# Optimization experiments

Hardware: AMD Instinct MI355X
Metric: run time of the kernel (lower is better)

The kernel has to match this reference:

```python
import jax, jax.numpy as jnp
import numpy as np

B, R, C, E, H = 2, 190, 512, 256, 8  # batch, pair-rows, alignment cols, embed, heads
D = E // H  # head_dim = 32; head_qk_dim = 1 since qk_dim == nb_heads


def setup_inputs() -> dict:
    key = jax.random.key(0)
    ks = jax.random.split(key, 6)
    s = 0.02
    return {
        "x": jax.random.normal(ks[0], (B, R, C, E), dtype=jnp.float32),
        "Wq": jax.random.normal(ks[1], (H, E), dtype=jnp.float32) * s,
        "bq": jnp.zeros((H,), dtype=jnp.float32),
        "Wk": jax.random.normal(ks[2], (H, E), dtype=jnp.float32) * s,
        "bk": jnp.zeros((H,), dtype=jnp.float32),
        "Wv": jax.random.normal(ks[3], (E, E), dtype=jnp.float32) * s,
        "bv": jnp.zeros((E,), dtype=jnp.float32),
        "Wo": jax.random.normal(ks[4], (E, E), dtype=jnp.float32) * s,
        "bo": jnp.zeros((E,), dtype=jnp.float32),
    }


def reference(x, Wq, bq, Wk, bk, Wv, bv, Wo, bo):
    b, r, c, e = x.shape
    h = Wq.shape[0]
    d = e // h
    # q,k projections: qk_dim == nb_heads, so per-head qk feature dim is 1.
    # Shapes: [b,r,h,c] (head axis before the col axis, matching transpose(2,3)).
    q = jnp.einsum('brce,he->brhc', x, Wq) + bq[:, None]
    k = jnp.einsum('brce,he->brhc', x, Wk) + bk[:, None]
    # v: [b,r,h,c,d]
    v = (jnp.einsum('brce,fe->brcf', x, Wv) + bv).reshape(b, r, c, h, d)
    v = jnp.transpose(v, (0, 1, 3, 2, 4))
    # elu+1 feature map, then normalize over the col (sequence) axis
    q = jax.nn.elu(q) + 1.0
    k = jax.nn.elu(k) + 1.0
    q = q / jnp.mean(q, axis=-1, keepdims=True)
    k = k / jnp.sum(k, axis=-1, keepdims=True)
    # KtV: k^T @ v with qk head-dim 1 -> [b,r,h,d]
    ktv = jnp.einsum('brhc,brhcd->brhd', k, v)
    # q @ KtV -> [b,r,c,h,d], flatten heads back to embed dim
    V = jnp.einsum('brhc,brhd->brchd', q, ktv).reshape(b, r, c, e)
    out = jnp.einsum('brce,fe->brcf', V, Wo) + bo
    return out
```

## Files before the change

kernel.cpp:

```cpp
#include <hip/hip_runtime.h>
#include <stdint.h>

#define PAIRS  380
#define CDIM   512
#define EDIM   256
#define HDIM   8
#define DDIM   32
#define CHUNK  64
#define NCHUNK 8
#define XSTR   260
#define NSPLIT 4
#define CPS    2

#define Q_OFF      0
#define MSH_OFF    4096
#define YP_OFF     6144
#define QS_OFF     14336
#define KS_OFF     14368
#define SCR_FLOATS 14400
#define OUT_STRIDE 131072

__device__ __forceinline__ float bf2f(uint16_t u) {
  union { uint32_t i; float f; } v; v.i = ((uint32_t)u) << 16; return v.f;
}
__device__ __forceinline__ uint16_t f2bf(float f) {
  union { float f; uint32_t i; } v; v.f = f;
  return (uint16_t)((v.i + 0x7FFFu + ((v.i >> 16) & 1u)) >> 16);
}

__device__ __forceinline__ float4 ld4(const void* p, size_t idx, int f32) {
  if (f32) return ((const float4*)p)[idx >> 2];
  ushort4 u = *(const ushort4*)((const uint16_t*)p + idx);
  return make_float4(bf2f(u.x), bf2f(u.y), bf2f(u.z), bf2f(u.w));
}
__device__ __forceinline__ float ld1(const void* p, size_t idx, int f32) {
  return f32 ? ((const float*)p)[idx] : bf2f(((const uint16_t*)p)[idx]);
}

__global__ void sniff_all(const uint16_t* p0, const uint16_t* p1, const uint16_t* p2,
                          const uint16_t* p3, const uint16_t* p4, const uint16_t* p5,
                          const uint16_t* p6, const uint16_t* p7, const uint16_t* p8,
                          int n0, int n1, int n2, int n3, int n4, int n5, int n6,
                          int n7, int n8, int* __restrict__ flags) {
  const uint16_t* ps[9] = {p0, p1, p2, p3, p4, p5, p6, p7, p8};
  const int       ns[9] = {n0, n1, n2, n3, n4, n5, n6, n7, n8};
  __shared__ int sf;
  const int tid = threadIdx.x;
  #pragma unroll
  for (int j = 0; j < 9; ++j) {
    if (tid == 0) sf = 0;
    __syncthreads();
    const uint16_t* p = ps[j];
    int lim = ns[j] < 4096 ? ns[j] : 4096;
    int huge = 0;
    for (int i = tid; i < lim; i += 256) {
      int e = (p[i] >> 7) & 0xFF;
      huge |= (e >= 0xA0);
    }
    if (huge) atomicOr(&sf, 1);
    __syncthreads();
    if (tid == 0) flags[j] = sf;
    __syncthreads();
  }
}

__global__ void __launch_bounds__(256, 2)
sla_phase1(const void* __restrict__ xg,
           const void* __restrict__ Wq, const void* __restrict__ bq,
           const void* __restrict__ Wk, const void* __restrict__ bk,
           const int* __restrict__ flags,
           float* __restrict__ scratch, long long sstride)
{
  const int fx = flags[0], fwq = flags[1], fbq = flags[2];
  const int fwk = flags[3], fbk = flags[4];

  __shared__ __align__(16) uint16_t xs[CHUNK][XSTR];
  __shared__ __align__(16) float    wqk[16][EDIM];
  __shared__ __align__(16) float    kc[CHUNK][HDIM];

  const int tid  = threadIdx.x;
  const int pair = blockIdx.x / NSPLIT;
  const int sp   = blockIdx.x % NSPLIT;
  const size_t xbase = (size_t)pair * (CDIM * EDIM);
  float* sbase = scratch + (size_t)pair * (size_t)sstride;

  for (int i = tid; i < 16 * EDIM / 4; i += 256) {
    int row = i >> 6;
    int col = (i & 63) << 2;
    float4 w = (row < 8) ? ld4(Wq, (size_t)row * EDIM + col, fwq)
                         : ld4(Wk, (size_t)(row - 8) * EDIM + col, fwk);
    *(float4*)&wqk[row][col] = w;
  }

  const int t  = tid >> 6;
  const int cl = tid & 63;
  const int h0 = (t & 1) * 4;
  const void* bsrc = (t < 2) ? bq : bk;
  const int   fb   = (t < 2) ? fbq : fbk;
  const float bias0 = ld1(bsrc, h0 + 0, fb), bias1 = ld1(bsrc, h0 + 1, fb),
              bias2 = ld1(bsrc, h0 + 2, fb), bias3 = ld1(bsrc, h0 + 3, fb);

  float yreg[HDIM] = {0.f,0.f,0.f,0.f,0.f,0.f,0.f,0.f};
  float cs0 = 0.f, cs1 = 0.f, cs2 = 0.f, cs3 = 0.f;

  for (int ci = 0; ci < CPS; ++ci) {
    const int cbase = (sp * CPS + ci) * CHUNK;
    __syncthreads();
    #pragma unroll
    for (int i = 0; i < 16; ++i) {
      int u  = i * 256 + tid;
      int c  = u >> 6;
      int e4 = (u & 63) << 2;
      float4 xv = ld4(xg, xbase + (size_t)(cbase + c) * EDIM + e4, fx);
      ushort4 s; s.x = f2bf(xv.x); s.y = f2bf(xv.y); s.z = f2bf(xv.z); s.w = f2bf(xv.w);
      *(ushort4*)&xs[c][e4] = s;
    }
    __syncthreads();
    {
      float a0 = bias0, a1 = bias1, a2 = bias2, a3 = bias3;
      const int r0 = t * 4;
      #pragma unroll 4
      for (int e = 0; e < EDIM; e += 4) {
        ushort4 xv = *(const ushort4*)&xs[cl][e];
        float x0 = bf2f(xv.x), x1 = bf2f(xv.y), x2 = bf2f(xv.z), x3 = bf2f(xv.w);
        float4 w0 = *(const float4*)&wqk[r0 + 0][e];
        float4 w1 = *(const float4*)&wqk[r0 + 1][e];
        float4 w2 = *(const float4*)&wqk[r0 + 2][e];
        float4 w3 = *(const float4*)&wqk[r0 + 3][e];
        a0 += x0 * w0.x + x1 * w0.y + x2 * w0.z + x3 * w0.w;
        a1 += x0 * w1.x + x1 * w1.y + x2 * w1.z + x3 * w1.w;
        a2 += x0 * w2.x + x1 * w2.y + x2 * w2.z + x3 * w2.w;
        a3 += x0 * w3.x + x1 * w3.y + x2 * w3.z + x3 * w3.w;
      }
      a0 = (a0 > 0.f) ? a0 + 1.f : __expf(a0);
      a1 = (a1 > 0.f) ? a1 + 1.f : __expf(a1);
      a2 = (a2 > 0.f) ? a2 + 1.f : __expf(a2);
      a3 = (a3 > 0.f) ? a3 + 1.f : __expf(a3);
      cs0 += a0; cs1 += a1; cs2 += a2; cs3 += a3;
      if (t < 2) *(float4*)&sbase[Q_OFF + (size_t)(cbase + cl) * HDIM + h0]
                   = make_float4(a0, a1, a2, a3);
      else       *(float4*)&kc[cl][h0] = make_float4(a0, a1, a2, a3);
    }
    __syncthreads();
    #pragma unroll 8
    for (int c = 0; c < CHUNK; ++c) {
      float xv = bf2f(xs[c][tid]);
      float4 k0 = *(const float4*)&kc[c][0];
      float4 k1 = *(const float4*)&kc[c][4];
      yreg[0] += k0.x * xv; yreg[1] += k0.y * xv; yreg[2] += k0.z * xv; yreg[3] += k0.w * xv;
      yreg[4] += k1.x * xv; yreg[5] += k1.y * xv; yreg[6] += k1.z * xv; yreg[7] += k1.w * xv;
    }
  }

  #pragma unroll
  for (int off = 32; off >= 1; off >>= 1) {
    cs0 += __shfl_xor(cs0, off, 64);
    cs1 += __shfl_xor(cs1, off, 64);
    cs2 += __shfl_xor(cs2, off, 64);
    cs3 += __shfl_xor(cs3, off, 64);
  }
  if ((tid & 63) == 0) {
    if (t < 2) *(float4*)&sbase[QS_OFF + sp * HDIM + h0] = make_float4(cs0, cs1, cs2, cs3);
    else       *(float4*)&sbase[KS_OFF + sp * HDIM + h0] = make_float4(cs0, cs1, cs2, cs3);
  }

  float* yp = sbase + YP_OFF + (size_t)sp * (HDIM * EDIM);
  #pragma unroll
  for (int h = 0; h < HDIM; ++h) yp[h * EDIM + tid] = yreg[h];
}

__global__ void __launch_bounds__(256, 2)
sla_phase2(const void* __restrict__ Wv, const void* __restrict__ bv,
           const void* __restrict__ Wo,
           const int* __restrict__ flags,
           float* __restrict__ scratch, long long sstride)
{
  const int fwv = flags[5], fbv = flags[6], fwo = flags[7];
  __shared__ __align__(16) float ysh[HDIM][EDIM];
  __shared__ __align__(16) float ktv[HDIM][DDIM];
  __shared__ float sQ[HDIM], sK[HDIM];
  const int tid = threadIdx.x;
  float* sbase = scratch + (size_t)blockIdx.x * (size_t)sstride;

  if (tid < 16) {
    int h = tid & 7;
    const float* ps = sbase + ((tid < 8) ? QS_OFF : KS_OFF);
    float s = 0.f;
    #pragma unroll
    for (int sp = 0; sp < NSPLIT; ++sp) s += ps[sp * HDIM + h];
    if (tid < 8) sQ[h] = 512.f / s;
    else         sK[h] = 1.f / s;
  }
  __syncthreads();

  {
    const float* yp = sbase + YP_OFF;
    #pragma unroll
    for (int h = 0; h < HDIM; ++h) {
      float y = 0.f;
      #pragma unroll
      for (int sp = 0; sp < NSPLIT; ++sp) y += yp[(sp * HDIM + h) * EDIM + tid];
      ysh[h][tid] = y * sK[h];
    }
  }
  __syncthreads();

  {
    const int h = tid >> 5, d = tid & 31;
    const size_t wvrow = (size_t)(h * DDIM + d) * EDIM;
    float acc = 0.f;
    #pragma unroll 4
    for (int e = 0; e < EDIM; e += 8) {
      float4 wa = ld4(Wv, wvrow + e, fwv);
      float4 wb = ld4(Wv, wvrow + e + 4, fwv);
      float4 ya = *(const float4*)&ysh[h][e];
      float4 yb = *(const float4*)&ysh[h][e + 4];
      acc += wa.x * ya.x + wa.y * ya.y + wa.z * ya.z + wa.w * ya.w
           + wb.x * yb.x + wb.y * yb.y + wb.z * yb.z + wb.w * yb.w;
    }
    ktv[h][d] = acc + ld1(bv, h * DDIM + d, fbv);
  }
  __syncthreads();

  {
    const int f = tid;
    const size_t worow = (size_t)f * EDIM;
    float* msh = sbase + MSH_OFF;
    #pragma unroll
    for (int h = 0; h < HDIM; ++h) {
      float m = 0.f;
      #pragma unroll
      for (int d = 0; d < DDIM; d += 8) {
        float4 wa = ld4(Wo, worow + h * DDIM + d, fwo);
        float4 wb = ld4(Wo, worow + h * DDIM + d + 4, fwo);
        float4 ka = *(const float4*)&ktv[h][d];
        float4 kb = *(const float4*)&ktv[h][d + 4];
        m += wa.x * ka.x + wa.y * ka.y + wa.z * ka.z + wa.w * ka.w
           + wb.x * kb.x + wb.y * kb.y + wb.z * kb.z + wb.w * kb.w;
      }
      msh[h * EDIM + f] = m * sQ[h];
    }
  }
}

__global__ void __launch_bounds__(256, 2)
sla_phase3(const float* __restrict__ scratch, long long sstride,
           const void* __restrict__ bo, const int* __restrict__ flags,
           float* __restrict__ outg, int shift)
{
  const int fbo = flags[8];
  __shared__ __align__(16) float qsh[CDIM][HDIM];
  __shared__ __align__(16) float msh[HDIM][EDIM];
  const int tid  = threadIdx.x;
  const int pair = blockIdx.x >> shift;
  const int seg  = blockIdx.x & ((1 << shift) - 1);
  const int rows = CDIM >> shift;
  const int c0   = seg * rows;
  const float* sbase = scratch + (size_t)pair * (size_t)sstride;

  for (int i = tid; i < rows * HDIM / 4; i += 256) {
    *(float4*)&qsh[i >> 1][(i & 1) * 4] =
        *(const float4*)&sbase[Q_OFF + (size_t)c0 * HDIM + (size_t)i * 4];
  }
  {
    const float* mp = sbase + MSH_OFF;
    for (int i = tid; i < HDIM * EDIM / 4; i += 256) {
      *(float4*)((float*)msh + (size_t)i * 4) = *(const float4*)&mp[(size_t)i * 4];
    }
  }
  __syncthreads();

  const int fq = tid & 63, cg = tid >> 6;
  const int f0 = fq * 4;
  float M[HDIM][4];
  #pragma unroll
  for (int h = 0; h < HDIM; ++h) {
    float4 mm = *(const float4*)&msh[h][f0];
    M[h][0] = mm.x; M[h][1] = mm.y; M[h][2] = mm.z; M[h][3] = mm.w;
  }
  const float b0 = ld1(bo, f0 + 0, fbo), b1 = ld1(bo, f0 + 1, fbo),
              b2 = ld1(bo, f0 + 2, fbo), b3 = ld1(bo, f0 + 3, fbo);
  float* outp = outg + (size_t)pair * OUT_STRIDE;
  const int rpw = rows >> 2;
  for (int i = 0; i < rpw; ++i) {
    int c = cg * rpw + i;
    float4 qa = *(const float4*)&qsh[c][0];
    float4 qb = *(const float4*)&qsh[c][4];
    float o0 = b0 + qa.x * M[0][0] + qa.y * M[1][0] + qa.z * M[2][0] + qa.w * M[3][0]
                  + qb.x * M[4][0] + qb.y * M[5][0] + qb.z * M[6][0] + qb.w * M[7][0];
    float o1 = b1 + qa.x * M[0][1] + qa.y * M[1][1] + qa.z * M[2][1] + qa.w * M[3][1]
                  + qb.x * M[4][1] + qb.y * M[5][1] + qb.z * M[6][1] + qb.w * M[7][1];
    float o2 = b2 + qa.x * M[0][2] + qa.y * M[1][2] + qa.z * M[2][2] + qa.w * M[3][2]
                  + qb.x * M[4][2] + qb.y * M[5][2] + qb.z * M[6][2] + qb.w * M[7][2];
    float o3 = b3 + qa.x * M[0][3] + qa.y * M[1][3] + qa.z * M[2][3] + qa.w * M[3][3]
                  + qb.x * M[4][3] + qb.y * M[5][3] + qb.z * M[6][3] + qb.w * M[7][3];
    *(float4*)(outp + (size_t)(c0 + c) * EDIM + f0) = make_float4(o0, o1, o2, o3);
  }
}

extern "C" void kernel_launch(void* const* d_in, const int* in_sizes, int n_in,
                              void* d_out, int out_size, void* d_ws, size_t ws_size,
                              hipStream_t stream) {
  (void)n_in; (void)out_size;
  int* flags = (int*)d_ws;
  hipLaunchKernelGGL(sniff_all, dim3(1), dim3(256), 0, stream,
                     (const uint16_t*)d_in[0], (const uint16_t*)d_in[1],
                     (const uint16_t*)d_in[2], (const uint16_t*)d_in[3],
                     (const uint16_t*)d_in[4], (const uint16_t*)d_in[5],
                     (const uint16_t*)d_in[6], (const uint16_t*)d_in[7],
                     (const uint16_t*)d_in[8],
                     in_sizes[0], in_sizes[1], in_sizes[2], in_sizes[3], in_sizes[4],
                     in_sizes[5], in_sizes[6], in_sizes[7], in_sizes[8], flags);

  const size_t need = 256 + (size_t)PAIRS * SCR_FLOATS * sizeof(float);
  float*    scratch;
  long long sstride;
  int       shift;
  if (ws_size >= need) {
    scratch = (float*)((char*)d_ws + 256);
    sstride = SCR_FLOATS;
    shift   = 2;
  } else {
    scratch = (float*)d_out;
    sstride = OUT_STRIDE;
    shift   = 0;
  }

  hipLaunchKernelGGL(sla_phase1, dim3(PAIRS * NSPLIT), dim3(256), 0, stream,
                     d_in[0], d_in[1], d_in[2], d_in[3], d_in[4],
                     (const int*)flags, scratch, sstride);
  hipLaunchKernelGGL(sla_phase2, dim3(PAIRS), dim3(256), 0, stream,
                     d_in[5], d_in[6], d_in[7], (const int*)flags, scratch, sstride);
  hipLaunchKernelGGL(sla_phase3, dim3(PAIRS << shift), dim3(256), 0, stream,
                     scratch, sstride, d_in[8], (const int*)flags,
                     (float*)d_out, shift);
}
```

Baseline: 482.1 us.

## Restructure phase1: pre-packed QK weights, swizzled LDS, finer column split

Phase1 now splits each pair into 8 single-chunk blocks instead of 4 blocks of two chunks each, and raises its occupancy hint from 2 to 4 blocks. The sniff kernel converts Wq/Wk and their biases to fp32 once, so blocks read the weights from global/L2 instead of staging them in LDS. x is copied into a XOR-swizzled LDS tile using 16-byte bf16 loads when the input is bf16. The projection loop has each thread compute two columns for two heads, and the K^T·x accumulation is split across 4 row groups and reduced through LDS. This trades more scratch partials and an extra reduction for less LDS use and better load efficiency. In the fallback path the packed weights are placed inside the output buffer, which risks aliasing with scratch data there.

```diff
diff --git a/kernel.cpp b/kernel.cpp
--- a/kernel.cpp
+++ b/kernel.cpp
@@ -7,18 +7,19 @@
 #define HDIM   8
 #define DDIM   32
 #define CHUNK  64
-#define NCHUNK 8
-#define XSTR   260
-#define NSPLIT 4
-#define CPS    2
+#define NSPLIT 8
 
 #define Q_OFF      0
 #define MSH_OFF    4096
 #define YP_OFF     6144
-#define QS_OFF     14336
-#define KS_OFF     14368
-#define SCR_FLOATS 14400
+#define QS_OFF     22528
+#define KS_OFF     22592
+#define SCR_FLOATS 22656
 #define OUT_STRIDE 131072
+
+#define WS_CW_OFF   1024
+#define WS_CB_OFF   17408
+#define WS_SCR_OFF  32768
 
 __device__ __forceinline__ float bf2f(uint16_t u) {
   union { uint32_t i; float f; } v; v.i = ((uint32_t)u) << 16; return v.f;
@@ -26,6 +27,12 @@
 __device__ __forceinline__ uint16_t f2bf(float f) {
   union { float f; uint32_t i; } v; v.f = f;
   return (uint16_t)((v.i + 0x7FFFu + ((v.i >> 16) & 1u)) >> 16);
+}
+__device__ __forceinline__ float blo(uint32_t u) {
+  union { uint32_t i; float f; } v; v.i = u << 16; return v.f;
+}
+__device__ __forceinline__ float bhi(uint32_t u) {
+  union { uint32_t i; float f; } v; v.i = u & 0xFFFF0000u; return v.f;
 }
 
 __device__ __forceinline__ float4 ld4(const void* p, size_t idx, int f32) {
@@ -37,14 +44,16 @@
   return f32 ? ((const float*)p)[idx] : bf2f(((const uint16_t*)p)[idx]);
 }
 
-__global__ void sniff_all(const uint16_t* p0, const uint16_t* p1, const uint16_t* p2,
-                          const uint16_t* p3, const uint16_t* p4, const uint16_t* p5,
-                          const uint16_t* p6, const uint16_t* p7, const uint16_t* p8,
-                          int n0, int n1, int n2, int n3, int n4, int n5, int n6,
-                          int n7, int n8, int* __restrict__ flags) {
+__global__ void sniff_pack(const uint16_t* p0, const uint16_t* p1, const uint16_t* p2,
+                           const uint16_t* p3, const uint16_t* p4, const uint16_t* p5,
+                           const uint16_t* p6, const uint16_t* p7, const uint16_t* p8,
+                           int n0, int n1, int n2, int n3, int n4, int n5, int n6,
+                           int n7, int n8, int* __restrict__ flags,
+                           float* __restrict__ cw, float* __restrict__ cb) {
   const uint16_t* ps[9] = {p0, p1, p2, p3, p4, p5, p6, p7, p8};
   const int       ns[9] = {n0, n1, n2, n3, n4, n5, n6, n7, n8};
   __shared__ int sf;
+  __shared__ int sflags[9];
   const int tid = threadIdx.x;
   #pragma unroll
   for (int j = 0; j < 9; ++j) {
@@ -59,114 +68,145 @@
     }
     if (huge) atomicOr(&sf, 1);
     __syncthreads();
-    if (tid == 0) flags[j] = sf;
+    if (tid == 0) { flags[j] = sf; sflags[j] = sf; }
     __syncthreads();
   }
-}
-
-__global__ void __launch_bounds__(256, 2)
+  for (int i = tid; i < 16 * EDIM; i += 256) {
+    int r = i >> 8, c = i & 255;
+    cw[i] = (r < 8) ? ld1(p1, (size_t)r * EDIM + c, sflags[1])
+                    : ld1(p3, (size_t)(r - 8) * EDIM + c, sflags[3]);
+  }
+  if (tid < 8)       cb[tid] = ld1(p2, tid, sflags[2]);
+  else if (tid < 16) cb[tid] = ld1(p4, tid - 8, sflags[4]);
+}
+
+__global__ void __launch_bounds__(256, 4)
 sla_phase1(const void* __restrict__ xg,
-           const void* __restrict__ Wq, const void* __restrict__ bq,
-           const void* __restrict__ Wk, const void* __restrict__ bk,
+           const float* __restrict__ cw, const float* __restrict__ cb,
            const int* __restrict__ flags,
            float* __restrict__ scratch, long long sstride)
 {
-  const int fx = flags[0], fwq = flags[1], fbq = flags[2];
-  const int fwk = flags[3], fbk = flags[4];
-
-  __shared__ __align__(16) uint16_t xs[CHUNK][XSTR];
-  __shared__ __align__(16) float    wqk[16][EDIM];
+  const int fx = flags[0];
+  __shared__ __align__(16) uint16_t xs[CHUNK][256];
   __shared__ __align__(16) float    kc[CHUNK][HDIM];
 
-  const int tid  = threadIdx.x;
-  const int pair = blockIdx.x / NSPLIT;
-  const int sp   = blockIdx.x % NSPLIT;
-  const size_t xbase = (size_t)pair * (CDIM * EDIM);
+  const int tid   = threadIdx.x;
+  const int pair  = blockIdx.x >> 3;
+  const int sp    = blockIdx.x & 7;
+  const int cbase = sp * CHUNK;
+  const size_t xelem = ((size_t)pair * CDIM + cbase) * EDIM;
   float* sbase = scratch + (size_t)pair * (size_t)sstride;
-
-  for (int i = tid; i < 16 * EDIM / 4; i += 256) {
-    int row = i >> 6;
-    int col = (i & 63) << 2;
-    float4 w = (row < 8) ? ld4(Wq, (size_t)row * EDIM + col, fwq)
-                         : ld4(Wk, (size_t)(row - 8) * EDIM + col, fwk);
-    *(float4*)&wqk[row][col] = w;
-  }
-
-  const int t  = tid >> 6;
-  const int cl = tid & 63;
-  const int h0 = (t & 1) * 4;
-  const void* bsrc = (t < 2) ? bq : bk;
-  const int   fb   = (t < 2) ? fbq : fbk;
-  const float bias0 = ld1(bsrc, h0 + 0, fb), bias1 = ld1(bsrc, h0 + 1, fb),
-              bias2 = ld1(bsrc, h0 + 2, fb), bias3 = ld1(bsrc, h0 + 3, fb);
-
-  float yreg[HDIM] = {0.f,0.f,0.f,0.f,0.f,0.f,0.f,0.f};
-  float cs0 = 0.f, cs1 = 0.f, cs2 = 0.f, cs3 = 0.f;
-
-  for (int ci = 0; ci < CPS; ++ci) {
-    const int cbase = (sp * CPS + ci) * CHUNK;
-    __syncthreads();
+  char*  xb    = (char*)&xs[0][0];
+
+  if (!fx) {
+    const uint4* xp = (const uint4*)xg + (xelem >> 3);
+    #pragma unroll
+    for (int i = 0; i < 8; ++i) {
+      int u = i * 256 + tid;
+      int c = u >> 5, s = u & 31;
+      uint4 v = xp[u];
+      *(uint4*)(xb + c * 512 + ((s ^ (c & 7)) << 4)) = v;
+    }
+  } else {
+    const float4* xp = (const float4*)xg + (xelem >> 2);
     #pragma unroll
     for (int i = 0; i < 16; ++i) {
-      int u  = i * 256 + tid;
-      int c  = u >> 6;
-      int e4 = (u & 63) << 2;
-      float4 xv = ld4(xg, xbase + (size_t)(cbase + c) * EDIM + e4, fx);
-      ushort4 s; s.x = f2bf(xv.x); s.y = f2bf(xv.y); s.z = f2bf(xv.z); s.w = f2bf(xv.w);
-      *(ushort4*)&xs[c][e4] = s;
-    }
-    __syncthreads();
-    {
-      float a0 = bias0, a1 = bias1, a2 = bias2, a3 = bias3;
-      const int r0 = t * 4;
-      #pragma unroll 4
-      for (int e = 0; e < EDIM; e += 4) {
-        ushort4 xv = *(const ushort4*)&xs[cl][e];
-        float x0 = bf2f(xv.x), x1 = bf2f(xv.y), x2 = bf2f(xv.z), x3 = bf2f(xv.w);
-        float4 w0 = *(const float4*)&wqk[r0 + 0][e];
-        float4 w1 = *(const float4*)&wqk[r0 + 1][e];
-        float4 w2 = *(const float4*)&wqk[r0 + 2][e];
-        float4 w3 = *(const float4*)&wqk[r0 + 3][e];
-        a0 += x0 * w0.x + x1 * w0.y + x2 * w0.z + x3 * w0.w;
-        a1 += x0 * w1.x + x1 * w1.y + x2 * w1.z + x3 * w1.w;
-        a2 += x0 * w2.x + x1 * w2.y + x2 * w2.z + x3 * w2.w;
-        a3 += x0 * w3.x + x1 * w3.y + x2 * w3.z + x3 * w3.w;
-      }
-      a0 = (a0 > 0.f) ? a0 + 1.f : __expf(a0);
-      a1 = (a1 > 0.f) ? a1 + 1.f : __expf(a1);
-      a2 = (a2 > 0.f) ? a2 + 1.f : __expf(a2);
-      a3 = (a3 > 0.f) ? a3 + 1.f : __expf(a3);
-      cs0 += a0; cs1 += a1; cs2 += a2; cs3 += a3;
-      if (t < 2) *(float4*)&sbase[Q_OFF + (size_t)(cbase + cl) * HDIM + h0]
-                   = make_float4(a0, a1, a2, a3);
-      else       *(float4*)&kc[cl][h0] = make_float4(a0, a1, a2, a3);
-    }
-    __syncthreads();
-    #pragma unroll 8
-    for (int c = 0; c < CHUNK; ++c) {
-      float xv = bf2f(xs[c][tid]);
-      float4 k0 = *(const float4*)&kc[c][0];
-      float4 k1 = *(const float4*)&kc[c][4];
-      yreg[0] += k0.x * xv; yreg[1] += k0.y * xv; yreg[2] += k0.z * xv; yreg[3] += k0.w * xv;
-      yreg[4] += k1.x * xv; yreg[5] += k1.y * xv; yreg[6] += k1.z * xv; yreg[7] += k1.w * xv;
-    }
-  }
-
-  #pragma unroll
-  for (int off = 32; off >= 1; off >>= 1) {
+      int u = i * 256 + tid;
+      int c = u >> 6, q4 = u & 63;
+      float4 xv = xp[u];
+      ushort4 sv; sv.x = f2bf(xv.x); sv.y = f2bf(xv.y); sv.z = f2bf(xv.z); sv.w = f2bf(xv.w);
+      int s = q4 >> 1, half = q4 & 1;
+      *(ushort4*)(xb + c * 512 + ((s ^ (c & 7)) << 4) + (half << 3)) = sv;
+    }
+  }
+  __syncthreads();
+
+  const int g  = tid >> 5;
+  const int l  = tid & 31;
+  const int wr = (g < 4) ? (g << 1) : (8 + ((g - 4) << 1));
+  const int h0 = (g & 3) << 1;
+  const float* w0 = cw + (size_t)wr * EDIM;
+  const float* w1 = w0 + EDIM;
+  float a00 = cb[wr], a01 = cb[wr + 1];
+  float a10 = cb[wr], a11 = cb[wr + 1];
+  const char* xr0 = xb + l * 512;
+  const char* xr1 = xr0 + 32 * 512;
+  const int   sw  = l & 7;
+
+  #pragma unroll 8
+  for (int s = 0; s < 32; ++s) {
+    uint4 xl = *(const uint4*)(xr0 + ((s ^ sw) << 4));
+    uint4 xh = *(const uint4*)(xr1 + ((s ^ sw) << 4));
+    float4 wa = *(const float4*)(w0 + s * 8);
+    float4 wb = *(const float4*)(w0 + s * 8 + 4);
+    float4 wc = *(const float4*)(w1 + s * 8);
+    float4 wd = *(const float4*)(w1 + s * 8 + 4);
+    float x0 = blo(xl.x), x1 = bhi(xl.x), x2 = blo(xl.y), x3 = bhi(xl.y);
+    float x4 = blo(xl.z), x5 = bhi(xl.z), x6 = blo(xl.w), x7 = bhi(xl.w);
+    a00 += x0*wa.x + x1*wa.y + x2*wa.z + x3*wa.w + x4*wb.x + x5*wb.y + x6*wb.z + x7*wb.w;
+    a01 += x0*wc.x + x1*wc.y + x2*wc.z + x3*wc.w + x4*wd.x + x5*wd.y + x6*wd.z + x7*wd.w;
+    float y0 = blo(xh.x), y1 = bhi(xh.x), y2 = blo(xh.y), y3 = bhi(xh.y);
+    float y4 = blo(xh.z), y5 = bhi(xh.z), y6 = blo(xh.w), y7 = bhi(xh.w);
+    a10 += y0*wa.x + y1*wa.y + y2*wa.z + y3*wa.w + y4*wb.x + y5*wb.y + y6*wb.z + y7*wb.w;
+    a11 += y0*wc.x + y1*wc.y + y2*wc.z + y3*wc.w + y4*wd.x + y5*wd.y + y6*wd.z + y7*wd.w;
+  }
+  a00 = (a00 > 0.f) ? a00 + 1.f : __expf(a00);
+  a01 = (a01 > 0.f) ? a01 + 1.f : __expf(a01);
+  a10 = (a10 > 0.f) ? a10 + 1.f : __expf(a10);
+  a11 = (a11 > 0.f) ? a11 + 1.f : __expf(a11);
+  float cs0 = a00 + a10, cs1 = a01 + a11;
+
+  if (g < 4) {
+    *(float2*)&sbase[Q_OFF + (size_t)(cbase + l) * 8 + h0]      = make_float2(a00, a01);
+    *(float2*)&sbase[Q_OFF + (size_t)(cbase + l + 32) * 8 + h0] = make_float2(a10, a11);
+  } else {
+    *(float2*)&kc[l][h0]      = make_float2(a00, a01);
+    *(float2*)&kc[l + 32][h0] = make_float2(a10, a11);
+  }
+  __syncthreads();
+
+  const int rg = tid >> 6, c4 = (tid & 63) << 2;
+  const int sy = c4 >> 3, hy = (c4 >> 2) & 1;
+  float yr[HDIM][4];
+  #pragma unroll
+  for (int h = 0; h < HDIM; ++h) { yr[h][0] = 0.f; yr[h][1] = 0.f; yr[h][2] = 0.f; yr[h][3] = 0.f; }
+  #pragma unroll 4
+  for (int i = 0; i < 16; ++i) {
+    int r = (rg << 4) + i;
+    ushort4 xv = *(const ushort4*)(xb + r * 512 + ((sy ^ (r & 7)) << 4) + (hy << 3));
+    float x0 = bf2f(xv.x), x1 = bf2f(xv.y), x2 = bf2f(xv.z), x3 = bf2f(xv.w);
+    float4 k0 = *(const float4*)&kc[r][0];
+    float4 k1 = *(const float4*)&kc[r][4];
+    float kh[8] = {k0.x, k0.y, k0.z, k0.w, k1.x, k1.y, k1.z, k1.w};
+    #pragma unroll
+    for (int h = 0; h < HDIM; ++h) {
+      yr[h][0] += kh[h] * x0; yr[h][1] += kh[h] * x1;
+      yr[h][2] += kh[h] * x2; yr[h][3] += kh[h] * x3;
+    }
+  }
+  __syncthreads();
+  float* ovl = (float*)xb;
+  #pragma unroll
+  for (int h = 0; h < HDIM; ++h)
+    *(float4*)&ovl[((rg << 3) + h) * 256 + c4] = make_float4(yr[h][0], yr[h][1], yr[h][2], yr[h][3]);
+  __syncthreads();
+  float* yp = sbase + YP_OFF + (size_t)sp * (HDIM * EDIM);
+  #pragma unroll
+  for (int h = 0; h < HDIM; ++h) {
+    float v = ovl[h * 256 + tid] + ovl[(8 + h) * 256 + tid]
+            + ovl[(16 + h) * 256 + tid] + ovl[(24 + h) * 256 + tid];
+    yp[h * EDIM + tid] = v;
+  }
+
+  #pragma unroll
+  for (int off = 16; off >= 1; off >>= 1) {
     cs0 += __shfl_xor(cs0, off, 64);
     cs1 += __shfl_xor(cs1, off, 64);
-    cs2 += __shfl_xor(cs2, off, 64);
-    cs3 += __shfl_xor(cs3, off, 64);
-  }
-  if ((tid & 63) == 0) {
-    if (t < 2) *(float4*)&sbase[QS_OFF + sp * HDIM + h0] = make_float4(cs0, cs1, cs2, cs3);
-    else       *(float4*)&sbase[KS_OFF + sp * HDIM + h0] = make_float4(cs0, cs1, cs2, cs3);
-  }
-
-  float* yp = sbase + YP_OFF + (size_t)sp * (HDIM * EDIM);
-  #pragma unroll
-  for (int h = 0; h < HDIM; ++h) yp[h * EDIM + tid] = yreg[h];
+  }
+  if ((tid & 31) == 0) {
+    if (g < 4) *(float2*)&sbase[QS_OFF + sp * HDIM + h0] = make_float2(cs0, cs1);
+    else       *(float2*)&sbase[KS_OFF + sp * HDIM + h0] = make_float2(cs0, cs1);
+  }
 }
 
 __global__ void __launch_bounds__(256, 2)
@@ -303,31 +343,39 @@
                               hipStream_t stream) {
   (void)n_in; (void)out_size;
   int* flags = (int*)d_ws;
-  hipLaunchKernelGGL(sniff_all, dim3(1), dim3(256), 0, stream,
+
+  const size_t need = WS_SCR_OFF + (size_t)PAIRS * SCR_FLOATS * sizeof(float);
+  float*    scratch;
+  float*    cw;
+  float*    cb;
+  long long sstride;
+  int       shift;
+  if (ws_size >= need) {
+    cw      = (float*)((char*)d_ws + WS_CW_OFF);
+    cb      = (float*)((char*)d_ws + WS_CB_OFF);
+    scratch = (float*)((char*)d_ws + WS_SCR_OFF);
+    sstride = SCR_FLOATS;
+    shift   = 2;
+  } else {
+    scratch = (float*)d_out;
+    sstride = OUT_STRIDE;
+    shift   = 0;
+    cw = (float*)d_out + (size_t)(PAIRS - 1) * OUT_STRIDE + 65536;
+    cb = cw + 16 * EDIM;
+  }
+
+  hipLaunchKernelGGL(sniff_pack, dim3(1), dim3(256), 0, stream,
                      (const uint16_t*)d_in[0], (const uint16_t*)d_in[1],
                      (const uint16_t*)d_in[2], (const uint16_t*)d_in[3],
                      (const uint16_t*)d_in[4], (const uint16_t*)d_in[5],
                      (const uint16_t*)d_in[6], (const uint16_t*)d_in[7],
                      (const uint16_t*)d_in[8],
                      in_sizes[0], in_sizes[1], in_sizes[2], in_sizes[3], in_sizes[4],
-                     in_sizes[5], in_sizes[6], in_sizes[7], in_sizes[8], flags);
-
-  const size_t need = 256 + (size_t)PAIRS * SCR_FLOATS * sizeof(float);
-  float*    scratch;
-  long long sstride;
-  int       shift;
-  if (ws_size >= need) {
-    scratch = (float*)((char*)d_ws + 256);
-    sstride = SCR_FLOATS;
-    shift   = 2;
-  } else {
-    scratch = (float*)d_out;
-    sstride = OUT_STRIDE;
-    shift   = 0;
-  }
+                     in_sizes[5], in_sizes[6], in_sizes[7], in_sizes[8], flags,
+                     cw, cb);
 
   hipLaunchKernelGGL(sla_phase1, dim3(PAIRS * NSPLIT), dim3(256), 0, stream,
-                     d_in[0], d_in[1], d_in[2], d_in[3], d_in[4],
+                     d_in[0], (const float*)cw, (const float*)cb,
                      (const int*)flags, scratch, sstride);
   hipLaunchKernelGGL(sla_phase2, dim3(PAIRS), dim3(256), 0, stream,
                      d_in[5], d_in[6], d_in[7], (const int*)flags, scratch, sstride);
```

New measurement: 488.5 us. No clear change (+1.3%).
